# Performance work log

Hardware: AMD Instinct MI355X
Metric: run time of the kernel (lower is better)

## Reference

```python
import jax, jax.numpy as jnp
import numpy as np
from jax import lax

N, D, NUM_SPEC, NUM_HOPS = 8192, 256, 32, 3
ETA, EPS, LN_EPS = 0.5, 0.5, 1e-5


def setup_inputs() -> dict:
    key = jax.random.key(0)
    ks = jax.random.split(key, 4)
    H = jax.random.normal(ks[0], (N, D), dtype=jnp.float32)
    # normalized adjacency proxy: scale so spectral norm is O(1) and hops stay stable
    A = jax.random.normal(ks[1], (N, N), dtype=jnp.float32) / jnp.sqrt(jnp.float32(N))
    # orthonormal-ish eigenvector columns
    V = jax.random.normal(ks[2], (N, NUM_SPEC), dtype=jnp.float32)
    V = V / jnp.linalg.norm(V, axis=0, keepdims=True)
    eigvals = jax.random.uniform(ks[3], (NUM_SPEC,), dtype=jnp.float32, maxval=2.0)
    return {
        "H": H,
        "A": A,
        "V": V,
        "eigvals": eigvals,
        "spec_logits": jnp.zeros((NUM_SPEC,), jnp.float32),
        "lap_logits": jnp.full((NUM_SPEC,), 0.1, jnp.float32),
        "hop_weights": jnp.full((NUM_HOPS + 1,), 1.0 / (NUM_HOPS + 1), jnp.float32),
        "threshold": jnp.full((D,), 0.05, jnp.float32),
        "ln_gamma": jnp.ones((D,), jnp.float32),
        "ln_beta": jnp.zeros((D,), jnp.float32),
    }


def reference(H, A, V, eigvals, spec_logits, lap_logits, hop_weights, threshold, ln_gamma, ln_beta):
    n, d = H.shape
    num_hops = hop_weights.shape[0] - 1

    # hop propagation: hops[k] = A^k H, shape [K, n, d] with K = num_hops+1
    def step(Hc, _):
        Hn = A @ Hc
        return Hn, Hn
    _, rest = lax.scan(step, H, None, length=num_hops)
    hops = jnp.concatenate([H[None], rest], axis=0)  # [K, n, d]

    hop_w = jax.nn.softmax(hop_weights)          # [K]
    spec_w = jax.nn.softmax(spec_logits)         # [S]
    lap_lams = jax.nn.softplus(lap_logits)       # [S]
    coeff = jnp.float32(d) / (jnp.float32(n) * jnp.float32(EPS) ** 2)

    # Phi[k,s,:] = v_s^T H_k  -> batched rank-1 projections
    Phi = jnp.einsum('ns,knd->ksd', V, hops)     # [K, S, d]

    # M = I + coeff * phi phi^T, batched small [d,d] SPD solves
    eye = jnp.eye(d, dtype=H.dtype)
    M = eye + coeff * jnp.einsum('ksi,ksj->ksij', Phi, Phi)  # [K,S,d,d]
    # phi @ M^{-1} == M^{-1} phi (M symmetric)
    q = coeff * jnp.linalg.solve(M, Phi[..., None])[..., 0]  # [K,S,d]

    # grad_R_total = sum_{k,s} hop_w[k] spec_w[s] v_s q_{k,s}^T = V @ T_R
    T_R = spec_w[:, None] * jnp.einsum('k,ksd->sd', hop_w, q)       # [S,d]
    grad_R = V @ T_R                                                 # [n,d]

    # grad_L_total = sum_{k,s} hop_w[k] lap_lams[s] eig_s v_s phi_{k,s}^T
    T_L = (lap_lams * eigvals)[:, None] * jnp.einsum('k,ksd->sd', hop_w, Phi)
    grad_L = V @ T_L

    H_half = H + ETA * grad_R - ETA * grad_L

    # soft threshold (proximal L1)
    thr = threshold[None, :]
    H_out = jnp.sign(H_half) * jax.nn.relu(jnp.abs(H_half) - thr)

    # LayerNorm over last dim
    mu = jnp.mean(H_out, axis=-1, keepdims=True)
    var = jnp.var(H_out, axis=-1, keepdims=True)
    H_out = (H_out - mu) / jnp.sqrt(var + LN_EPS) * ln_gamma + ln_beta
    return (H_out, lax.stop_gradient(hop_w), lax.stop_gradient(spec_w))
```

## Files before the change

kernel.cpp:

```cpp
#include <hip/hip_runtime.h>
#include <hip/hip_bf16.h>
#include <stdint.h>

#define NN 8192
#define LDAT 8320
#define DIM 256
#define NSPEC 32
#define ETA 0.5f
#define COEFF 0.125f
#define LNEPS 1e-5f

typedef __attribute__((ext_vector_type(8))) short bf16x8;
typedef __attribute__((ext_vector_type(4))) float f32x4;
typedef __attribute__((ext_vector_type(4))) unsigned short u16x4;

__device__ __forceinline__ unsigned short bf2u(__hip_bfloat16 b) {
    union { __hip_bfloat16 b; unsigned short u; } c; c.b = b; return c.u;
}

__device__ __forceinline__ void async16(const void* g, void* l) {
    __builtin_amdgcn_global_load_lds(
        (const __attribute__((address_space(1))) void*)g,
        (__attribute__((address_space(3))) void*)l, 16, 0, 0);
}

__global__ void castT_A(const float* __restrict__ A, __hip_bfloat16* __restrict__ AT) {
    __shared__ unsigned short lds[64 * 72];
    const int t = threadIdx.x;
    const long r0 = (long)blockIdx.x * 64;
    const long c0 = (long)((blockIdx.x + blockIdx.y) & 127) * 64;
    const int rg = t >> 4;
    const int cg = t & 15;

    float4 a[4];
#pragma unroll
    for (int i = 0; i < 4; ++i)
        a[i] = *(const float4*)&A[(r0 + rg * 4 + i) * NN + c0 + cg * 4];

#pragma unroll
    for (int j = 0; j < 4; ++j) {
        u16x4 col;
        col[0] = bf2u(__float2bfloat16(((const float*)&a[0])[j]));
        col[1] = bf2u(__float2bfloat16(((const float*)&a[1])[j]));
        col[2] = bf2u(__float2bfloat16(((const float*)&a[2])[j]));
        col[3] = bf2u(__float2bfloat16(((const float*)&a[3])[j]));
        int c = cg * 4 + j;
        int s = (((rg >> 1) + cg) & 7) * 2 + (rg & 1);
        *(u16x4*)&lds[c * 72 + s * 4] = col;
    }
    __syncthreads();

#pragma unroll
    for (int i = 0; i < 2; ++i) {
        int idx = i * 256 + t;
        int c = idx >> 3, g = idx & 7;
        int s8 = (g + (c >> 2)) & 7;
        bf16x8 v = *(const bf16x8*)&lds[c * 72 + s8 * 8];
        *(bf16x8*)&AT[(c0 + c) * LDAT + r0 + g * 8] = v;
    }
}

__global__ void trans_V(const float* __restrict__ V, __hip_bfloat16* __restrict__ VT) {
    __shared__ float tile[64 * 33];
    int n0 = blockIdx.x * 64;
    int t = threadIdx.x;
    for (int i = 0; i < 8; ++i) {
        int idx = i * 256 + t;
        tile[(idx >> 5) * 33 + (idx & 31)] = V[(long)(n0 + (idx >> 5)) * NSPEC + (idx & 31)];
    }
    __syncthreads();
    for (int i = 0; i < 8; ++i) {
        int idx = i * 256 + t;
        int s = idx >> 6, r = idx & 63;
        VT[(long)s * NN + n0 + r] = __float2bfloat16(tile[r * 33 + s]);
    }
}

#define BM 128
#define BKH 128
#define HSPLIT 8
#define HKC (NN / HSPLIT)
#define HITERS (HKC / BKH)

__launch_bounds__(256, 2)
__global__ void gemm_hopW(const __hip_bfloat16* __restrict__ AT,
                          const __hip_bfloat16* __restrict__ WT,
                          float* __restrict__ P) {
    __shared__ __align__(16) __hip_bfloat16 As[2][BM * BKH];
    __shared__ __align__(16) __hip_bfloat16 Ws[2][NSPEC * BKH];
    const int t = threadIdx.x;
    const int w = t >> 6, l = t & 63;
    const int wm = w & 1, wn = w >> 1;
    const long gm0 = (long)blockIdx.x * BM;
    const long kbase = (long)blockIdx.y * HKC;

    const int lr4 = l >> 4;
    const int lg = l & 15;

    auto stage = [&](int buf, long kpos) {
#pragma unroll
        for (int c = 0; c < 8; ++c) {
            int rb = w * 32 + c * 4;
            int row = rb + lr4;
            async16(AT + (gm0 + row) * (long)LDAT + kpos + ((lg ^ (row & 15)) << 3),
                    &As[buf][rb * BKH]);
        }
#pragma unroll
        for (int c = 0; c < 2; ++c) {
            int rb = w * 8 + c * 4;
            int row = rb + lr4;
            async16(WT + (long)row * NN + kpos + ((lg ^ (row & 15)) << 3),
                    &Ws[buf][rb * BKH]);
        }
    };

    f32x4 acc[4];
#pragma unroll
    for (int mt = 0; mt < 4; ++mt) acc[mt] = (f32x4){0.f, 0.f, 0.f, 0.f};

    const int rowq = l & 15;
    const int kq = l >> 4;

    stage(0, kbase);
    for (int kt = 0; kt < HITERS; ++kt) {
        __syncthreads();
        const int cur = kt & 1;
        if (kt + 1 < HITERS) stage(cur ^ 1, kbase + (long)(kt + 1) * BKH);

#pragma unroll
        for (int ks = 0; ks < 4; ++ks) {
            const int pg = ((ks * 4 + kq) ^ rowq) << 3;
            bf16x8 bfrag = *(const bf16x8*)&Ws[cur][(wn * 16 + rowq) * BKH + pg];
#pragma unroll
            for (int mt = 0; mt < 4; ++mt) {
                bf16x8 afrag = *(const bf16x8*)&As[cur][(wm * 64 + mt * 16 + rowq) * BKH + pg];
                acc[mt] = __builtin_amdgcn_mfma_f32_16x16x32_bf16(afrag, bfrag, acc[mt], 0, 0, 0);
            }
        }
    }

    float* Pz = P + (long)blockIdx.y * NN * NSPEC;
    const int s = wn * 16 + (l & 15);
#pragma unroll
    for (int mt = 0; mt < 4; ++mt)
#pragma unroll
        for (int r = 0; r < 4; ++r) {
            long m = gm0 + wm * 64 + mt * 16 + (l >> 4) * 4 + r;
            Pz[m * NSPEC + s] = acc[mt][r];
        }
}

__global__ void reduce_W(const float* __restrict__ P, float* __restrict__ Wf,
                         __hip_bfloat16* __restrict__ WTbf) {
    __shared__ float tile[64 * 33];
    int n0 = blockIdx.x * 64;
    int t = threadIdx.x;
    for (int i = 0; i < 8; ++i) {
        int idx = i * 256 + t;
        int r = idx >> 5, s = idx & 31;
        long off = (long)(n0 + r) * NSPEC + s;
        float v = 0.f;
#pragma unroll
        for (int z = 0; z < HSPLIT; ++z) v += P[(long)z * NN * NSPEC + off];
        Wf[off] = v;
        tile[r * 33 + s] = v;
    }
    __syncthreads();
    for (int i = 0; i < 8; ++i) {
        int idx = i * 256 + t;
        int s = idx >> 6, r = idx & 63;
        WTbf[(long)s * NN + n0 + r] = __float2bfloat16(tile[r * 33 + s]);
    }
}

__global__ void phi_kernel(const float* __restrict__ W0, const float* __restrict__ W1,
                           const float* __restrict__ W2, const float* __restrict__ W3,
                           const float* __restrict__ H, float* __restrict__ Phi) {
    __shared__ float ldsW[64 * NSPEC];
    int t = threadIdx.x;
    int s0 = (t >> 6) * 8;
    int d0 = (t & 63) * 4;
    int n0 = blockIdx.x * 128;
    int k = blockIdx.y;
    const float* W = (k == 0) ? W0 : (k == 1) ? W1 : (k == 2) ? W2 : W3;
    float4 acc[8];
#pragma unroll
    for (int j = 0; j < 8; ++j) acc[j] = (float4){0.f, 0.f, 0.f, 0.f};

    for (int tile = 0; tile < 2; ++tile) {
        int nb = n0 + tile * 64;
#pragma unroll
        for (int i = 0; i < 8; ++i) {
            int idx = i * 256 + t;
            ldsW[idx] = W[(long)(nb + (idx >> 5)) * NSPEC + (idx & 31)];
        }
        __syncthreads();
        for (int nn = 0; nn < 64; ++nn) {
            float4 x = *(const float4*)&H[(long)(nb + nn) * DIM + d0];
#pragma unroll
            for (int j = 0; j < 8; ++j) {
                float vs = ldsW[nn * NSPEC + s0 + j];
                acc[j].x += vs * x.x; acc[j].y += vs * x.y;
                acc[j].z += vs * x.z; acc[j].w += vs * x.w;
            }
        }
        __syncthreads();
    }
#pragma unroll
    for (int j = 0; j < 8; ++j) {
        float* ph = &Phi[((k * NSPEC) + s0 + j) * DIM + d0];
        atomicAdd(ph + 0, acc[j].x);
        atomicAdd(ph + 1, acc[j].y);
        atomicAdd(ph + 2, acc[j].z);
        atomicAdd(ph + 3, acc[j].w);
    }
}

__global__ void tc_kernel(const float* __restrict__ Phi,
                          const float* __restrict__ eigvals,
                          const float* __restrict__ spec_logits,
                          const float* __restrict__ lap_logits,
                          const float* __restrict__ hop_weights,
                          float* __restrict__ Tc,
                          float* __restrict__ out_tail) {
    int s = blockIdx.x, t = threadIdx.x;
    float hw0 = hop_weights[0], hw1 = hop_weights[1], hw2 = hop_weights[2], hw3 = hop_weights[3];
    float hm = fmaxf(fmaxf(hw0, hw1), fmaxf(hw2, hw3));
    hw0 = expf(hw0 - hm); hw1 = expf(hw1 - hm); hw2 = expf(hw2 - hm); hw3 = expf(hw3 - hm);
    float hs = hw0 + hw1 + hw2 + hw3;
    hw0 /= hs; hw1 /= hs; hw2 /= hs; hw3 /= hs;
    float hw[4] = {hw0, hw1, hw2, hw3};
    float sm = -1e30f;
    for (int j = 0; j < NSPEC; ++j) sm = fmaxf(sm, spec_logits[j]);
    float ssum = 0.f;
    for (int j = 0; j < NSPEC; ++j) ssum += expf(spec_logits[j] - sm);
    float spec_w_s = expf(spec_logits[s] - sm) / ssum;
    float lp = lap_logits[s];
    float lap = (lp > 20.f) ? lp : log1pf(expf(lp));
    float le = lap * eigvals[s];

    __shared__ float red[4];
    float accR = 0.f, accL = 0.f;
    for (int k = 0; k < 4; ++k) {
        float phi = Phi[(k * NSPEC + s) * DIM + t];
        float v = phi * phi;
        for (int off = 32; off; off >>= 1) v += __shfl_xor(v, off);
        if ((t & 63) == 0) red[t >> 6] = v;
        __syncthreads();
        float ssq = red[0] + red[1] + red[2] + red[3];
        __syncthreads();
        float q = COEFF * phi / (1.f + COEFF * ssq);
        accR += hw[k] * q;
        accL += hw[k] * phi;
    }
    Tc[s * DIM + t] = spec_w_s * accR - le * accL;
    if (s == 0) {
        if (t < 4) out_tail[t] = hw[t];
        if (t < NSPEC) out_tail[4 + t] = expf(spec_logits[t] - sm) / ssum;
    }
}

__launch_bounds__(256)
__global__ void final_kernel(const float* __restrict__ H, const float* __restrict__ V,
                             const float* __restrict__ Tc, const float* __restrict__ thr,
                             const float* __restrict__ gamma, const float* __restrict__ beta,
                             float* __restrict__ out) {
    __shared__ float tc[NSPEC * DIM];
    int t = threadIdx.x;
    {
        const float4* s4 = (const float4*)Tc;
        float4* d4 = (float4*)tc;
        for (int i = 0; i < 8; ++i) d4[i * 256 + t] = s4[i * 256 + t];
    }
    __syncthreads();
    int w = t >> 6, l = t & 63;
    long row = (long)blockIdx.x * 4 + w;
    int d0 = l * 4;
    const float* vrow = V + row * NSPEC;
    float4 G = {0.f, 0.f, 0.f, 0.f};
#pragma unroll 8
    for (int s = 0; s < NSPEC; ++s) {
        float vs = vrow[s];
        float4 c4 = *(const float4*)&tc[s * DIM + d0];
        G.x += vs * c4.x; G.y += vs * c4.y; G.z += vs * c4.z; G.w += vs * c4.w;
    }
    float4 h = *(const float4*)&H[row * DIM + d0];
    float4 th = *(const float4*)&thr[d0];
    float y[4];
    y[0] = h.x + ETA * G.x; y[1] = h.y + ETA * G.y;
    y[2] = h.z + ETA * G.z; y[3] = h.w + ETA * G.w;
    float tv[4] = {th.x, th.y, th.z, th.w};
    float s1 = 0.f, s2 = 0.f;
#pragma unroll
    for (int j = 0; j < 4; ++j) {
        float a = fabsf(y[j]) - tv[j];
        y[j] = (a > 0.f) ? copysignf(a, y[j]) : 0.f;
        s1 += y[j];
        s2 += y[j] * y[j];
    }
    for (int off = 32; off; off >>= 1) { s1 += __shfl_xor(s1, off); s2 += __shfl_xor(s2, off); }
    float mean = s1 * (1.f / DIM);
    float var = s2 * (1.f / DIM) - mean * mean;
    float inv = rsqrtf(var + LNEPS);
    float4 g4 = *(const float4*)&gamma[d0];
    float4 b4 = *(const float4*)&beta[d0];
    float4 o;
    o.x = (y[0] - mean) * inv * g4.x + b4.x;
    o.y = (y[1] - mean) * inv * g4.y + b4.y;
    o.z = (y[2] - mean) * inv * g4.z + b4.z;
    o.w = (y[3] - mean) * inv * g4.w + b4.w;
    *(float4*)&out[row * DIM + d0] = o;
}

extern "C" void kernel_launch(void* const* d_in, const int* in_sizes, int n_in,
                              void* d_out, int out_size, void* d_ws, size_t ws_size,
                              hipStream_t stream) {
    const float* H = (const float*)d_in[0];
    const float* A = (const float*)d_in[1];
    const float* V = (const float*)d_in[2];
    const float* eigvals = (const float*)d_in[3];
    const float* spec_logits = (const float*)d_in[4];
    const float* lap_logits = (const float*)d_in[5];
    const float* hop_weights = (const float*)d_in[6];
    const float* threshold = (const float*)d_in[7];
    const float* ln_gamma = (const float*)d_in[8];
    const float* ln_beta = (const float*)d_in[9];

    char* ws = (char*)d_ws;
    __hip_bfloat16* ATbf = (__hip_bfloat16*)ws;
    float*          P    = (float*)(ws + 136314880);
    __hip_bfloat16* VTbf = (__hip_bfloat16*)(ws + 144703488);
    float* W1f = (float*)(ws + 145227776);
    float* W2f = (float*)(ws + 146276352);
    float* W3f = (float*)(ws + 147324928);
    __hip_bfloat16* W1T = (__hip_bfloat16*)(ws + 148373504);
    __hip_bfloat16* W2T = (__hip_bfloat16*)(ws + 148897792);
    __hip_bfloat16* W3T = (__hip_bfloat16*)(ws + 149422080);
    float* Phi = (float*)(ws + 149946368);
    float* Tc  = (float*)(ws + 150077440);
    float* out = (float*)d_out;

    hipMemsetAsync(Phi, 0, 4 * NSPEC * DIM * sizeof(float), stream);
    castT_A<<<dim3(128, 128), 256, 0, stream>>>(A, ATbf);
    trans_V<<<128, 256, 0, stream>>>(V, VTbf);

    gemm_hopW<<<dim3(64, HSPLIT), 256, 0, stream>>>(ATbf, VTbf, P);
    reduce_W<<<128, 256, 0, stream>>>(P, W1f, W1T);
    gemm_hopW<<<dim3(64, HSPLIT), 256, 0, stream>>>(ATbf, W1T, P);
    reduce_W<<<128, 256, 0, stream>>>(P, W2f, W2T);
    gemm_hopW<<<dim3(64, HSPLIT), 256, 0, stream>>>(ATbf, W2T, P);
    reduce_W<<<128, 256, 0, stream>>>(P, W3f, W3T);

    phi_kernel<<<dim3(64, 4), 256, 0, stream>>>(V, W1f, W2f, W3f, H, Phi);
    tc_kernel<<<NSPEC, 256, 0, stream>>>(Phi, eigvals, spec_logits, lap_logits, hop_weights,
                                         Tc, out + (long)NN * DIM);
    final_kernel<<<2048, 256, 0, stream>>>(H, V, Tc, threshold, ln_gamma, ln_beta, out);
}
```

Before: 561.8 us.

## Replace LDS-staged hop GEMM with register-direct MFMA loads and wider K split

The skinny A^T·W GEMM no longer stages tiles through LDS with async loads and barriers. Each wave now loads its A and W fragments straight from global memory into registers, double-buffered, and computes a 64x32 output tile. The K split grows from 8 to 32 slices, which gives a 32x32 grid, and the partial-sum buffer is padded to spread the slices. The goal is to remove LDS traffic and syncs in this bandwidth-bound GEMM and to raise occupancy and parallelism. The cost is four times more partial-sum traffic in reduce_W and uncoalesced strided global fragment loads.

Result: slower. 593.0 us (+5.6%).

```diff
diff --git a/kernel.cpp b/kernel.cpp
--- a/kernel.cpp
+++ b/kernel.cpp
@@ -6,6 +6,10 @@
 #define LDAT 8320
 #define DIM 256
 #define NSPEC 32
+#define ZS 32
+#define KC (NN / ZS)
+#define NKS (KC / 32)
+#define PZSTRIDE (NN * NSPEC + 256)
 #define ETA 0.5f
 #define COEFF 0.125f
 #define LNEPS 1e-5f
@@ -16,12 +20,6 @@
 
 __device__ __forceinline__ unsigned short bf2u(__hip_bfloat16 b) {
     union { __hip_bfloat16 b; unsigned short u; } c; c.b = b; return c.u;
-}
-
-__device__ __forceinline__ void async16(const void* g, void* l) {
-    __builtin_amdgcn_global_load_lds(
-        (const __attribute__((address_space(1))) void*)g,
-        (__attribute__((address_space(3))) void*)l, 16, 0, 0);
 }
 
 __global__ void castT_A(const float* __restrict__ A, __hip_bfloat16* __restrict__ AT) {
@@ -76,78 +74,60 @@
     }
 }
 
-#define BM 128
-#define BKH 128
-#define HSPLIT 8
-#define HKC (NN / HSPLIT)
-#define HITERS (HKC / BKH)
-
-__launch_bounds__(256, 2)
-__global__ void gemm_hopW(const __hip_bfloat16* __restrict__ AT,
+__launch_bounds__(256, 4)
+__global__ void gemm_mfma(const __hip_bfloat16* __restrict__ AT,
                           const __hip_bfloat16* __restrict__ WT,
                           float* __restrict__ P) {
-    __shared__ __align__(16) __hip_bfloat16 As[2][BM * BKH];
-    __shared__ __align__(16) __hip_bfloat16 Ws[2][NSPEC * BKH];
     const int t = threadIdx.x;
-    const int w = t >> 6, l = t & 63;
-    const int wm = w & 1, wn = w >> 1;
-    const long gm0 = (long)blockIdx.x * BM;
-    const long kbase = (long)blockIdx.y * HKC;
-
-    const int lr4 = l >> 4;
-    const int lg = l & 15;
-
-    auto stage = [&](int buf, long kpos) {
-#pragma unroll
-        for (int c = 0; c < 8; ++c) {
-            int rb = w * 32 + c * 4;
-            int row = rb + lr4;
-            async16(AT + (gm0 + row) * (long)LDAT + kpos + ((lg ^ (row & 15)) << 3),
-                    &As[buf][rb * BKH]);
+    const int wv = t >> 6, l = t & 63;
+    const long n0 = (long)blockIdx.x * 256 + wv * 64;
+    const long kb = (long)blockIdx.y * KC;
+    const int lr = l & 15;
+    const int lk = (l >> 4) * 8;
+
+    const __hip_bfloat16* Ab = AT + (n0 + lr) * (long)LDAT + kb + lk;
+    const __hip_bfloat16* Bb = WT + (long)lr * NN + kb + lk;
+
+    bf16x8 af[2][4], bf[2][2];
+    f32x4 acc[4][2];
+#pragma unroll
+    for (int mt = 0; mt < 4; ++mt)
+#pragma unroll
+        for (int sb = 0; sb < 2; ++sb) acc[mt][sb] = (f32x4){0.f, 0.f, 0.f, 0.f};
+
+#pragma unroll
+    for (int mt = 0; mt < 4; ++mt) af[0][mt] = *(const bf16x8*)(Ab + (long)mt * 16 * LDAT);
+#pragma unroll
+    for (int sb = 0; sb < 2; ++sb) bf[0][sb] = *(const bf16x8*)(Bb + (long)sb * 16 * NN);
+
+#pragma unroll
+    for (int kk = 0; kk < NKS; ++kk) {
+        if (kk + 1 < NKS) {
+#pragma unroll
+            for (int mt = 0; mt < 4; ++mt)
+                af[(kk + 1) & 1][mt] = *(const bf16x8*)(Ab + (long)mt * 16 * LDAT + (kk + 1) * 32);
+#pragma unroll
+            for (int sb = 0; sb < 2; ++sb)
+                bf[(kk + 1) & 1][sb] = *(const bf16x8*)(Bb + (long)sb * 16 * NN + (kk + 1) * 32);
         }
 #pragma unroll
-        for (int c = 0; c < 2; ++c) {
-            int rb = w * 8 + c * 4;
-            int row = rb + lr4;
-            async16(WT + (long)row * NN + kpos + ((lg ^ (row & 15)) << 3),
-                    &Ws[buf][rb * BKH]);
-        }
-    };
-
-    f32x4 acc[4];
-#pragma unroll
-    for (int mt = 0; mt < 4; ++mt) acc[mt] = (f32x4){0.f, 0.f, 0.f, 0.f};
-
-    const int rowq = l & 15;
-    const int kq = l >> 4;
-
-    stage(0, kbase);
-    for (int kt = 0; kt < HITERS; ++kt) {
-        __syncthreads();
-        const int cur = kt & 1;
-        if (kt + 1 < HITERS) stage(cur ^ 1, kbase + (long)(kt + 1) * BKH);
-
-#pragma unroll
-        for (int ks = 0; ks < 4; ++ks) {
-            const int pg = ((ks * 4 + kq) ^ rowq) << 3;
-            bf16x8 bfrag = *(const bf16x8*)&Ws[cur][(wn * 16 + rowq) * BKH + pg];
-#pragma unroll
-            for (int mt = 0; mt < 4; ++mt) {
-                bf16x8 afrag = *(const bf16x8*)&As[cur][(wm * 64 + mt * 16 + rowq) * BKH + pg];
-                acc[mt] = __builtin_amdgcn_mfma_f32_16x16x32_bf16(afrag, bfrag, acc[mt], 0, 0, 0);
+        for (int mt = 0; mt < 4; ++mt)
+#pragma unroll
+            for (int sb = 0; sb < 2; ++sb)
+                acc[mt][sb] = __builtin_amdgcn_mfma_f32_16x16x32_bf16(
+                    af[kk & 1][mt], bf[kk & 1][sb], acc[mt][sb], 0, 0, 0);
+    }
+
+    float* Pz = P + (long)blockIdx.y * PZSTRIDE;
+#pragma unroll
+    for (int mt = 0; mt < 4; ++mt)
+#pragma unroll
+        for (int sb = 0; sb < 2; ++sb)
+#pragma unroll
+            for (int r = 0; r < 4; ++r) {
+                long n = n0 + mt * 16 + (l >> 4) * 4 + r;
+                Pz[n * NSPEC + sb * 16 + lr] = acc[mt][sb][r];
             }
-        }
-    }
-
-    float* Pz = P + (long)blockIdx.y * NN * NSPEC;
-    const int s = wn * 16 + (l & 15);
-#pragma unroll
-    for (int mt = 0; mt < 4; ++mt)
-#pragma unroll
-        for (int r = 0; r < 4; ++r) {
-            long m = gm0 + wm * 64 + mt * 16 + (l >> 4) * 4 + r;
-            Pz[m * NSPEC + s] = acc[mt][r];
-        }
 }
 
 __global__ void reduce_W(const float* __restrict__ P, float* __restrict__ Wf,
@@ -161,7 +141,7 @@
         long off = (long)(n0 + r) * NSPEC + s;
         float v = 0.f;
 #pragma unroll
-        for (int z = 0; z < HSPLIT; ++z) v += P[(long)z * NN * NSPEC + off];
+        for (int z = 0; z < ZS; ++z) v += P[(long)z * PZSTRIDE + off];
         Wf[off] = v;
         tile[r * 33 + s] = v;
     }
@@ -329,26 +309,26 @@
     char* ws = (char*)d_ws;
     __hip_bfloat16* ATbf = (__hip_bfloat16*)ws;
     float*          P    = (float*)(ws + 136314880);
-    __hip_bfloat16* VTbf = (__hip_bfloat16*)(ws + 144703488);
-    float* W1f = (float*)(ws + 145227776);
-    float* W2f = (float*)(ws + 146276352);
-    float* W3f = (float*)(ws + 147324928);
-    __hip_bfloat16* W1T = (__hip_bfloat16*)(ws + 148373504);
-    __hip_bfloat16* W2T = (__hip_bfloat16*)(ws + 148897792);
-    __hip_bfloat16* W3T = (__hip_bfloat16*)(ws + 149422080);
-    float* Phi = (float*)(ws + 149946368);
-    float* Tc  = (float*)(ws + 150077440);
+    __hip_bfloat16* VTbf = (__hip_bfloat16*)(ws + 169902080);
+    float* W1f = (float*)(ws + 170426368);
+    float* W2f = (float*)(ws + 171474944);
+    float* W3f = (float*)(ws + 172523520);
+    __hip_bfloat16* W1T = (__hip_bfloat16*)(ws + 173572096);
+    __hip_bfloat16* W2T = (__hip_bfloat16*)(ws + 174096384);
+    __hip_bfloat16* W3T = (__hip_bfloat16*)(ws + 174620672);
+    float* Phi = (float*)(ws + 175144960);
+    float* Tc  = (float*)(ws + 175276032);
     float* out = (float*)d_out;
 
     hipMemsetAsync(Phi, 0, 4 * NSPEC * DIM * sizeof(float), stream);
     castT_A<<<dim3(128, 128), 256, 0, stream>>>(A, ATbf);
     trans_V<<<128, 256, 0, stream>>>(V, VTbf);
 
-    gemm_hopW<<<dim3(64, HSPLIT), 256, 0, stream>>>(ATbf, VTbf, P);
+    gemm_mfma<<<dim3(32, ZS), 256, 0, stream>>>(ATbf, VTbf, P);
     reduce_W<<<128, 256, 0, stream>>>(P, W1f, W1T);
-    gemm_hopW<<<dim3(64, HSPLIT), 256, 0, stream>>>(ATbf, W1T, P);
+    gemm_mfma<<<dim3(32, ZS), 256, 0, stream>>>(ATbf, W1T, P);
     reduce_W<<<128, 256, 0, stream>>>(P, W2f, W2T);
-    gemm_hopW<<<dim3(64, HSPLIT), 256, 0, stream>>>(ATbf, W2T, P);
+    gemm_mfma<<<dim3(32, ZS), 256, 0, stream>>>(ATbf, W2T, P);
     reduce_W<<<128, 256, 0, stream>>>(P, W3f, W3T);
 
     phi_kernel<<<dim3(64, 4), 256, 0, stream>>>(V, W1f, W2f, W3f, H, Phi);
```
